# Kernel optimization log

Measured on AMD Instinct MI355X. Metric: run time of the kernel, lower is better.

## Reference

```python
import jax, jax.numpy as jnp
import numpy as np

B = 131072   # batch
K = 3        # kernel size (= stride)
NP = 9       # num patches (9x9 image, 3x3 kernel, stride 3)
NU = 81      # num logic units/kernels
NOPS = 16    # real-valued binary logic ops


def setup_inputs() -> dict:
    key = jax.random.key(0)
    k1, k2, k3, k4 = jax.random.split(key, 4)
    x = jax.random.uniform(k1, (B, 1, 9, 9), dtype=jnp.float32)          # soft-binary image
    sel_a_logits = jax.random.normal(k2, (NU, K * K), dtype=jnp.float32)  # input-A selector per unit
    sel_b_logits = jax.random.normal(k3, (NU, K * K), dtype=jnp.float32)  # input-B selector per unit
    op_logits = jax.random.normal(k4, (NU, NOPS), dtype=jnp.float32)      # logic-op mixture per unit
    return {"x": x, "sel_a_logits": sel_a_logits, "sel_b_logits": sel_b_logits, "op_logits": op_logits}


def _soft_logic_mix(a, b, w):
    # a, b: [B, NU] soft-binary operands; w: [NU, 16] op mixture weights (broadcast over batch).
    # The 16 real-valued binary logic gates (Petersen et al. differentiable logic networks).
    ab = a * b
    return (w[:, 1] * ab
            + w[:, 2] * (a - ab)
            + w[:, 3] * a
            + w[:, 4] * (b - ab)
            + w[:, 5] * b
            + w[:, 6] * (a + b - 2.0 * ab)      # xor
            + w[:, 7] * (a + b - ab)            # or
            + w[:, 8] * (1.0 - (a + b - ab))    # nor
            + w[:, 9] * (1.0 - (a + b - 2.0 * ab))  # xnor
            + w[:, 10] * (1.0 - b)
            + w[:, 11] * (1.0 - b + ab)
            + w[:, 12] * (1.0 - a)
            + w[:, 13] * (1.0 - a + ab)
            + w[:, 14] * (1.0 - ab)             # nand
            + w[:, 15])                          # op 0 contributes 0


def reference(x, sel_a_logits, sel_b_logits, op_logits):
    b_sz = x.shape[0]
    img = x[:, 0]  # [B, 9, 9]
    # unfold(2,K,S).unfold(3,K,S) with S == K == 3 -> non-overlapping 3x3 patches, row-major patch order
    patches = img.reshape(b_sz, NP // K, K, NP // K, K)
    patches = patches.transpose(0, 1, 3, 2, 4).reshape(b_sz, NP, K * K)  # [B, 9, 9]
    # unit u uses patch u // kernels_per_pos (kernels_per_pos = 81 // 9 = 9)
    unit2patch = jnp.arange(NU) // (NU // NP)
    inp = patches[:, unit2patch]  # [B, 81, 9]
    a = jnp.einsum('bui,ui->bu', inp, jax.nn.softmax(sel_a_logits, axis=-1))  # [B, 81]
    b = jnp.einsum('bui,ui->bu', inp, jax.nn.softmax(sel_b_logits, axis=-1))  # [B, 81]
    w = jax.nn.softmax(op_logits, axis=-1)  # [81, 16]
    return _soft_logic_mix(a, b, w)  # [B, 81]
```

## Files before the change

### kernel.cpp

```cpp
#include <hip/hip_runtime.h>
#include <math.h>


#define NB      131072
#define NUNITS  81
#define BPB     64
#define THREADS 256
#define NTILES  (NB / BPB)
#define PBLK    1792
#define REC     24
#define CHUNKS  (BPB * 81 / 4)

typedef __attribute__((address_space(1))) const void GAS;
typedef __attribute__((address_space(3))) void LAS;
typedef float vfloat4 __attribute__((ext_vector_type(4)));

__global__ __launch_bounds__(256)
void logic_prep_kernel(const float* __restrict__ sa_logits,
                       const float* __restrict__ sb_logits,
                       const float* __restrict__ op_logits,
                       float* __restrict__ tab)
{
    const int tid = threadIdx.x;
    if (tid < 81) {
        const int u = tid;
        float v[9], m = -1e30f;
        #pragma unroll
        for (int i = 0; i < 9; ++i) { v[i] = sa_logits[u * 9 + i]; m = fmaxf(m, v[i]); }
        float s = 0.f;
        #pragma unroll
        for (int i = 0; i < 9; ++i) { v[i] = expf(v[i] - m); s += v[i]; }
        const float r = 1.f / s;
        #pragma unroll
        for (int i = 0; i < 9; ++i) tab[u * REC + i] = v[i] * r;
    } else if (tid < 162) {
        const int u = tid - 81;
        float v[9], m = -1e30f;
        #pragma unroll
        for (int i = 0; i < 9; ++i) { v[i] = sb_logits[u * 9 + i]; m = fmaxf(m, v[i]); }
        float s = 0.f;
        #pragma unroll
        for (int i = 0; i < 9; ++i) { v[i] = expf(v[i] - m); s += v[i]; }
        const float r = 1.f / s;
        #pragma unroll
        for (int i = 0; i < 9; ++i) tab[u * REC + 9 + i] = v[i] * r;
    } else if (tid < 243) {
        const int u = tid - 162;
        float v[16], m = -1e30f;
        #pragma unroll
        for (int i = 0; i < 16; ++i) { v[i] = op_logits[u * 16 + i]; m = fmaxf(m, v[i]); }
        float s = 0.f;
        #pragma unroll
        for (int i = 0; i < 16; ++i) { v[i] = expf(v[i] - m); s += v[i]; }
        const float r = 1.f / s;
        #pragma unroll
        for (int i = 0; i < 16; ++i) v[i] *= r;
        const float cab = v[1] - v[2] - v[4] - 2.f*v[6] - v[7] + v[8] + 2.f*v[9]
                        + v[11] + v[13] - v[14];
        const float ca  = v[2] + v[3] + v[6] + v[7] - v[8] - v[9] - v[12] - v[13];
        const float cb  = v[4] + v[5] + v[6] + v[7] - v[8] - v[9] - v[10] - v[11];
        const float c0  = v[8] + v[9] + v[10] + v[11] + v[12] + v[13] + v[14] + v[15];
        tab[u * REC + 18] = cab;
        tab[u * REC + 19] = ca;
        tab[u * REC + 20] = cb;
        tab[u * REC + 21] = c0;
    }
}

__global__ __launch_bounds__(THREADS, 7)
void logic_main_kernel(const float* __restrict__ x,
                       const float* __restrict__ tab,
                       float* __restrict__ out)
{
    __shared__ float s_tile[BPB * 81];

    const int tid   = threadIdx.x;
    const int lane  = tid & 63;
    const int wavei = __builtin_amdgcn_readfirstlane(tid >> 6);

    for (int t = blockIdx.x; t < NTILES; t += PBLK) {
        const size_t b0 = (size_t)t * BPB;

        {
            const float4* gsrc = (const float4*)(x + b0 * 81);
            #pragma unroll
            for (int k = 0; k < 6; ++k) {
                const int j = tid + k * THREADS;
                if (j < CHUNKS) {
                    float* lbase = s_tile + (size_t)(k * THREADS + wavei * 64) * 4;
                    __builtin_amdgcn_global_load_lds((GAS*)(gsrc + j), (LAS*)lbase,
                                                     16, 0, 0);
                }
            }
        }
        __syncthreads();

        if (wavei < 3) {
            float* my = s_tile + lane * 81 + wavei * 27;

            float in[27];
            #pragma unroll
            for (int j = 0; j < 27; ++j) in[j] = my[j];

            const float4* __restrict__ wt4 =
                (const float4*)(tab + (size_t)wavei * 27 * REC);

            #pragma unroll
            for (int j = 0; j < 27; ++j) {
                const int q = j / 9;
                const float4 q0 = wt4[j * 6 + 0];
                const float4 q1 = wt4[j * 6 + 1];
                const float4 q2 = wt4[j * 6 + 2];
                const float4 q3 = wt4[j * 6 + 3];
                const float4 q4 = wt4[j * 6 + 4];
                const float4 q5 = wt4[j * 6 + 5];
                const float wa[9] = { q0.x, q0.y, q0.z, q0.w, q1.x, q1.y, q1.z, q1.w, q2.x };
                const float wb[9] = { q2.y, q2.z, q2.w, q3.x, q3.y, q3.z, q3.w, q4.x, q4.y };
                float a = 0.f, b = 0.f;
                #pragma unroll
                for (int i = 0; i < 9; ++i) {
                    const float xi = in[q * 3 + (i / 3) * 9 + (i % 3)];
                    a = fmaf(xi, wa[i], a);
                    b = fmaf(xi, wb[i], b);
                }
                my[j] = fmaf(q4.z, a * b, fmaf(q4.w, a, fmaf(q5.x, b, q5.y)));
            }
        }

        __syncthreads();

        {
            const vfloat4* s4 = (const vfloat4*)s_tile;
            vfloat4* gdst = (vfloat4*)(out + b0 * 81);
            #pragma unroll
            for (int k = 0; k < 6; ++k) {
                const int j = tid + k * THREADS;
                if (j < CHUNKS) __builtin_nontemporal_store(s4[j], gdst + j);
            }
        }

        __syncthreads();
    }
}

extern "C" void kernel_launch(void* const* d_in, const int* in_sizes, int n_in,
                              void* d_out, int out_size, void* d_ws, size_t ws_size,
                              hipStream_t stream)
{
    const float* x  = (const float*)d_in[0];
    const float* sa = (const float*)d_in[1];
    const float* sb = (const float*)d_in[2];
    const float* op = (const float*)d_in[3];
    float* tab  = (float*)d_ws;
    float* outp = (float*)d_out;

    logic_prep_kernel<<<1, 256, 0, stream>>>(sa, sb, op, tab);
    logic_main_kernel<<<PBLK, THREADS, 0, stream>>>(x, tab, outp);
}
```

Before: 26.37 us.

## Fuse softmax prep into main kernel with flag-based cross-block sync

Merges the single-block table-prep kernel into the main kernel. Block 0 computes the softmax table and publishes it via a release-store flag, while every block issues its input tile load first and then spins on the flag before computing. The goal is to hide one kernel-launch boundary and the prep latency behind the input load. The cost is an extra memset on the stream, a spin-wait that relies on block 0 being scheduled, and a hardcoded tile assignment (last 256 blocks take a second tile) that only works for the fixed NTILES/PBLK values.

After: 80.00 us. +203.3%, slower.

```diff
diff --git a/kernel.cpp b/kernel.cpp
--- a/kernel.cpp
+++ b/kernel.cpp
@@ -10,136 +10,165 @@
 #define PBLK    1792
 #define REC     24
 #define CHUNKS  (BPB * 81 / 4)
+#define TABF    (NUNITS * REC)
 
 typedef __attribute__((address_space(1))) const void GAS;
 typedef __attribute__((address_space(3))) void LAS;
 typedef float vfloat4 __attribute__((ext_vector_type(4)));
 
-__global__ __launch_bounds__(256)
-void logic_prep_kernel(const float* __restrict__ sa_logits,
-                       const float* __restrict__ sb_logits,
-                       const float* __restrict__ op_logits,
-                       float* __restrict__ tab)
+__device__ __forceinline__
+void stage_tile(const float* __restrict__ x, float* __restrict__ s_tile,
+                int tid, int wavei, size_t b0)
 {
-    const int tid = threadIdx.x;
-    if (tid < 81) {
-        const int u = tid;
-        float v[9], m = -1e30f;
+    const float4* gsrc = (const float4*)(x + b0 * 81);
+    #pragma unroll
+    for (int k = 0; k < 6; ++k) {
+        const int j = tid + k * THREADS;
+        if (j < CHUNKS) {
+            float* lbase = s_tile + (size_t)(k * THREADS + wavei * 64) * 4;
+            __builtin_amdgcn_global_load_lds((GAS*)(gsrc + j), (LAS*)lbase,
+                                             16, 0, 0);
+        }
+    }
+}
+
+__device__ __forceinline__
+void compute_tile(float* __restrict__ s_tile, const float* __restrict__ tab,
+                  int lane, int wavei)
+{
+    if (wavei < 3) {
+        float* my = s_tile + lane * 81 + wavei * 27;
+
+        float in[27];
         #pragma unroll
-        for (int i = 0; i < 9; ++i) { v[i] = sa_logits[u * 9 + i]; m = fmaxf(m, v[i]); }
-        float s = 0.f;
+        for (int j = 0; j < 27; ++j) in[j] = my[j];
+
+        const float4* __restrict__ wt4 =
+            (const float4*)(tab + (size_t)wavei * 27 * REC);
+
         #pragma unroll
-        for (int i = 0; i < 9; ++i) { v[i] = expf(v[i] - m); s += v[i]; }
-        const float r = 1.f / s;
-        #pragma unroll
-        for (int i = 0; i < 9; ++i) tab[u * REC + i] = v[i] * r;
-    } else if (tid < 162) {
-        const int u = tid - 81;
-        float v[9], m = -1e30f;
-        #pragma unroll
-        for (int i = 0; i < 9; ++i) { v[i] = sb_logits[u * 9 + i]; m = fmaxf(m, v[i]); }
-        float s = 0.f;
-        #pragma unroll
-        for (int i = 0; i < 9; ++i) { v[i] = expf(v[i] - m); s += v[i]; }
-        const float r = 1.f / s;
-        #pragma unroll
-        for (int i = 0; i < 9; ++i) tab[u * REC + 9 + i] = v[i] * r;
-    } else if (tid < 243) {
-        const int u = tid - 162;
-        float v[16], m = -1e30f;
-        #pragma unroll
-        for (int i = 0; i < 16; ++i) { v[i] = op_logits[u * 16 + i]; m = fmaxf(m, v[i]); }
-        float s = 0.f;
-        #pragma unroll
-        for (int i = 0; i < 16; ++i) { v[i] = expf(v[i] - m); s += v[i]; }
-        const float r = 1.f / s;
-        #pragma unroll
-        for (int i = 0; i < 16; ++i) v[i] *= r;
-        const float cab = v[1] - v[2] - v[4] - 2.f*v[6] - v[7] + v[8] + 2.f*v[9]
-                        + v[11] + v[13] - v[14];
-        const float ca  = v[2] + v[3] + v[6] + v[7] - v[8] - v[9] - v[12] - v[13];
-        const float cb  = v[4] + v[5] + v[6] + v[7] - v[8] - v[9] - v[10] - v[11];
-        const float c0  = v[8] + v[9] + v[10] + v[11] + v[12] + v[13] + v[14] + v[15];
-        tab[u * REC + 18] = cab;
-        tab[u * REC + 19] = ca;
-        tab[u * REC + 20] = cb;
-        tab[u * REC + 21] = c0;
+        for (int j = 0; j < 27; ++j) {
+            const int q = j / 9;
+            const float4 q0 = wt4[j * 6 + 0];
+            const float4 q1 = wt4[j * 6 + 1];
+            const float4 q2 = wt4[j * 6 + 2];
+            const float4 q3 = wt4[j * 6 + 3];
+            const float4 q4 = wt4[j * 6 + 4];
+            const float4 q5 = wt4[j * 6 + 5];
+            const float wa[9] = { q0.x, q0.y, q0.z, q0.w, q1.x, q1.y, q1.z, q1.w, q2.x };
+            const float wb[9] = { q2.y, q2.z, q2.w, q3.x, q3.y, q3.z, q3.w, q4.x, q4.y };
+            float a = 0.f, b = 0.f;
+            #pragma unroll
+            for (int i = 0; i < 9; ++i) {
+                const float xi = in[q * 3 + (i / 3) * 9 + (i % 3)];
+                a = fmaf(xi, wa[i], a);
+                b = fmaf(xi, wb[i], b);
+            }
+            my[j] = fmaf(q4.z, a * b, fmaf(q4.w, a, fmaf(q5.x, b, q5.y)));
+        }
+    }
+}
+
+__device__ __forceinline__
+void writeback_tile(const float* __restrict__ s_tile, float* __restrict__ out,
+                    int tid, size_t b0)
+{
+    const vfloat4* s4 = (const vfloat4*)s_tile;
+    vfloat4* gdst = (vfloat4*)(out + b0 * 81);
+    #pragma unroll
+    for (int k = 0; k < 6; ++k) {
+        const int j = tid + k * THREADS;
+        if (j < CHUNKS) __builtin_nontemporal_store(s4[j], gdst + j);
     }
 }
 
 __global__ __launch_bounds__(THREADS, 7)
-void logic_main_kernel(const float* __restrict__ x,
-                       const float* __restrict__ tab,
-                       float* __restrict__ out)
+void logic_all_kernel(const float* __restrict__ x,
+                      const float* __restrict__ sa_logits,
+                      const float* __restrict__ sb_logits,
+                      const float* __restrict__ op_logits,
+                      float* __restrict__ tab,
+                      int* __restrict__ flag,
+                      float* __restrict__ out)
 {
     __shared__ float s_tile[BPB * 81];
 
     const int tid   = threadIdx.x;
     const int lane  = tid & 63;
     const int wavei = __builtin_amdgcn_readfirstlane(tid >> 6);
+    const int bid   = blockIdx.x;
 
-    for (int t = blockIdx.x; t < NTILES; t += PBLK) {
-        const size_t b0 = (size_t)t * BPB;
-
-        {
-            const float4* gsrc = (const float4*)(x + b0 * 81);
+    if (bid == 0) {
+        if (tid < 81) {
+            const int u = tid;
+            float v[9], m = -1e30f;
             #pragma unroll
-            for (int k = 0; k < 6; ++k) {
-                const int j = tid + k * THREADS;
-                if (j < CHUNKS) {
-                    float* lbase = s_tile + (size_t)(k * THREADS + wavei * 64) * 4;
-                    __builtin_amdgcn_global_load_lds((GAS*)(gsrc + j), (LAS*)lbase,
-                                                     16, 0, 0);
-                }
-            }
+            for (int i = 0; i < 9; ++i) { v[i] = sa_logits[u * 9 + i]; m = fmaxf(m, v[i]); }
+            float s = 0.f;
+            #pragma unroll
+            for (int i = 0; i < 9; ++i) { v[i] = expf(v[i] - m); s += v[i]; }
+            const float r = 1.f / s;
+            #pragma unroll
+            for (int i = 0; i < 9; ++i) tab[u * REC + i] = v[i] * r;
+        } else if (tid < 162) {
+            const int u = tid - 81;
+            float v[9], m = -1e30f;
+            #pragma unroll
+            for (int i = 0; i < 9; ++i) { v[i] = sb_logits[u * 9 + i]; m = fmaxf(m, v[i]); }
+            float s = 0.f;
+            #pragma unroll
+            for (int i = 0; i < 9; ++i) { v[i] = expf(v[i] - m); s += v[i]; }
+            const float r = 1.f / s;
+            #pragma unroll
+            for (int i = 0; i < 9; ++i) tab[u * REC + 9 + i] = v[i] * r;
+        } else if (tid < 243) {
+            const int u = tid - 162;
+            float v[16], m = -1e30f;
+            #pragma unroll
+            for (int i = 0; i < 16; ++i) { v[i] = op_logits[u * 16 + i]; m = fmaxf(m, v[i]); }
+            float s = 0.f;
+            #pragma unroll
+            for (int i = 0; i < 16; ++i) { v[i] = expf(v[i] - m); s += v[i]; }
+            const float r = 1.f / s;
+            #pragma unroll
+            for (int i = 0; i < 16; ++i) v[i] *= r;
+            const float cab = v[1] - v[2] - v[4] - 2.f*v[6] - v[7] + v[8] + 2.f*v[9]
+                            + v[11] + v[13] - v[14];
+            const float ca  = v[2] + v[3] + v[6] + v[7] - v[8] - v[9] - v[12] - v[13];
+            const float cb  = v[4] + v[5] + v[6] + v[7] - v[8] - v[9] - v[10] - v[11];
+            const float c0  = v[8] + v[9] + v[10] + v[11] + v[12] + v[13] + v[14] + v[15];
+            tab[u * REC + 18] = cab;
+            tab[u * REC + 19] = ca;
+            tab[u * REC + 20] = cb;
+            tab[u * REC + 21] = c0;
         }
         __syncthreads();
+        if (tid == 0)
+            __hip_atomic_store(flag, 1, __ATOMIC_RELEASE, __HIP_MEMORY_SCOPE_AGENT);
+    }
 
-        if (wavei < 3) {
-            float* my = s_tile + lane * 81 + wavei * 27;
+    stage_tile(x, s_tile, tid, wavei, (size_t)bid * BPB);
+    __syncthreads();
 
-            float in[27];
-            #pragma unroll
-            for (int j = 0; j < 27; ++j) in[j] = my[j];
+    if (tid == 0) {
+        while (__hip_atomic_load(flag, __ATOMIC_ACQUIRE,
+                                 __HIP_MEMORY_SCOPE_AGENT) == 0)
+            __builtin_amdgcn_s_sleep(8);
+    }
+    __syncthreads();
 
-            const float4* __restrict__ wt4 =
-                (const float4*)(tab + (size_t)wavei * 27 * REC);
+    compute_tile(s_tile, tab, lane, wavei);
+    __syncthreads();
+    writeback_tile(s_tile, out, tid, (size_t)bid * BPB);
 
-            #pragma unroll
-            for (int j = 0; j < 27; ++j) {
-                const int q = j / 9;
-                const float4 q0 = wt4[j * 6 + 0];
-                const float4 q1 = wt4[j * 6 + 1];
-                const float4 q2 = wt4[j * 6 + 2];
-                const float4 q3 = wt4[j * 6 + 3];
-                const float4 q4 = wt4[j * 6 + 4];
-                const float4 q5 = wt4[j * 6 + 5];
-                const float wa[9] = { q0.x, q0.y, q0.z, q0.w, q1.x, q1.y, q1.z, q1.w, q2.x };
-                const float wb[9] = { q2.y, q2.z, q2.w, q3.x, q3.y, q3.z, q3.w, q4.x, q4.y };
-                float a = 0.f, b = 0.f;
-                #pragma unroll
-                for (int i = 0; i < 9; ++i) {
-                    const float xi = in[q * 3 + (i / 3) * 9 + (i % 3)];
-                    a = fmaf(xi, wa[i], a);
-                    b = fmaf(xi, wb[i], b);
-                }
-                my[j] = fmaf(q4.z, a * b, fmaf(q4.w, a, fmaf(q5.x, b, q5.y)));
-            }
-        }
-
+    if (bid >= PBLK - 256) {
         __syncthreads();
-
-        {
-            const vfloat4* s4 = (const vfloat4*)s_tile;
-            vfloat4* gdst = (vfloat4*)(out + b0 * 81);
-            #pragma unroll
-            for (int k = 0; k < 6; ++k) {
-                const int j = tid + k * THREADS;
-                if (j < CHUNKS) __builtin_nontemporal_store(s4[j], gdst + j);
-            }
-        }
-
+        const size_t b1 = (size_t)(bid + 256) * BPB;
+        stage_tile(x, s_tile, tid, wavei, b1);
         __syncthreads();
+        compute_tile(s_tile, tab, lane, wavei);
+        __syncthreads();
+        writeback_tile(s_tile, out, tid, b1);
     }
 }
 
@@ -152,8 +181,9 @@
     const float* sb = (const float*)d_in[2];
     const float* op = (const float*)d_in[3];
     float* tab  = (float*)d_ws;
+    int*   flag = (int*)((float*)d_ws + TABF);
     float* outp = (float*)d_out;
 
-    logic_prep_kernel<<<1, 256, 0, stream>>>(sa, sb, op, tab);
-    logic_main_kernel<<<PBLK, THREADS, 0, stream>>>(x, tab, outp);
+    hipMemsetAsync(flag, 0, sizeof(int), stream);
+    logic_all_kernel<<<PBLK, THREADS, 0, stream>>>(x, sa, sb, op, tab, flag, outp);
 }
```

## Fuse softmax prep into main kernel with per-block LDS weights and smaller tiles

Applied to the files above, without the earlier changes.

Drops the separate single-block prep kernel. Each block now computes the softmax selector and op-mixture coefficients itself into shared memory on its first tile, overlapping that work with the first tile's async global-to-LDS load. The batch tile shrinks from 64 to 48 rows, which gives 2731 tiles and a partial last tile. Weights are read from LDS instead of global memory. The cost is that every block recomputes the exp/softmax work, and the trailing barrier moves to the top of the loop.

Result: slower. 43.05 us (+63.2%).

```diff
diff --git a/kernel.cpp b/kernel.cpp
--- a/kernel.cpp
+++ b/kernel.cpp
@@ -4,126 +4,123 @@
 
 #define NB      131072
 #define NUNITS  81
-#define BPB     64
+#define BPB     48
 #define THREADS 256
-#define NTILES  (NB / BPB)
+#define NTILES  2731
 #define PBLK    1792
-#define REC     24
-#define CHUNKS  (BPB * 81 / 4)
+#define WREC    22
+#define LASTB   (NB - (NTILES - 1) * BPB)
 
 typedef __attribute__((address_space(1))) const void GAS;
 typedef __attribute__((address_space(3))) void LAS;
 typedef float vfloat4 __attribute__((ext_vector_type(4)));
 
-__global__ __launch_bounds__(256)
-void logic_prep_kernel(const float* __restrict__ sa_logits,
-                       const float* __restrict__ sb_logits,
-                       const float* __restrict__ op_logits,
-                       float* __restrict__ tab)
-{
-    const int tid = threadIdx.x;
-    if (tid < 81) {
-        const int u = tid;
-        float v[9], m = -1e30f;
-        #pragma unroll
-        for (int i = 0; i < 9; ++i) { v[i] = sa_logits[u * 9 + i]; m = fmaxf(m, v[i]); }
-        float s = 0.f;
-        #pragma unroll
-        for (int i = 0; i < 9; ++i) { v[i] = expf(v[i] - m); s += v[i]; }
-        const float r = 1.f / s;
-        #pragma unroll
-        for (int i = 0; i < 9; ++i) tab[u * REC + i] = v[i] * r;
-    } else if (tid < 162) {
-        const int u = tid - 81;
-        float v[9], m = -1e30f;
-        #pragma unroll
-        for (int i = 0; i < 9; ++i) { v[i] = sb_logits[u * 9 + i]; m = fmaxf(m, v[i]); }
-        float s = 0.f;
-        #pragma unroll
-        for (int i = 0; i < 9; ++i) { v[i] = expf(v[i] - m); s += v[i]; }
-        const float r = 1.f / s;
-        #pragma unroll
-        for (int i = 0; i < 9; ++i) tab[u * REC + 9 + i] = v[i] * r;
-    } else if (tid < 243) {
-        const int u = tid - 162;
-        float v[16], m = -1e30f;
-        #pragma unroll
-        for (int i = 0; i < 16; ++i) { v[i] = op_logits[u * 16 + i]; m = fmaxf(m, v[i]); }
-        float s = 0.f;
-        #pragma unroll
-        for (int i = 0; i < 16; ++i) { v[i] = expf(v[i] - m); s += v[i]; }
-        const float r = 1.f / s;
-        #pragma unroll
-        for (int i = 0; i < 16; ++i) v[i] *= r;
-        const float cab = v[1] - v[2] - v[4] - 2.f*v[6] - v[7] + v[8] + 2.f*v[9]
-                        + v[11] + v[13] - v[14];
-        const float ca  = v[2] + v[3] + v[6] + v[7] - v[8] - v[9] - v[12] - v[13];
-        const float cb  = v[4] + v[5] + v[6] + v[7] - v[8] - v[9] - v[10] - v[11];
-        const float c0  = v[8] + v[9] + v[10] + v[11] + v[12] + v[13] + v[14] + v[15];
-        tab[u * REC + 18] = cab;
-        tab[u * REC + 19] = ca;
-        tab[u * REC + 20] = cb;
-        tab[u * REC + 21] = c0;
-    }
-}
-
 __global__ __launch_bounds__(THREADS, 7)
-void logic_main_kernel(const float* __restrict__ x,
-                       const float* __restrict__ tab,
-                       float* __restrict__ out)
+void logic_fused_kernel(const float* __restrict__ x,
+                        const float* __restrict__ sa_logits,
+                        const float* __restrict__ sb_logits,
+                        const float* __restrict__ op_logits,
+                        float* __restrict__ out)
 {
     __shared__ float s_tile[BPB * 81];
+    __shared__ float s_w[NUNITS * WREC];
 
     const int tid   = threadIdx.x;
     const int lane  = tid & 63;
     const int wavei = __builtin_amdgcn_readfirstlane(tid >> 6);
+    const int bid   = blockIdx.x;
 
-    for (int t = blockIdx.x; t < NTILES; t += PBLK) {
-        const size_t b0 = (size_t)t * BPB;
+    bool first = true;
+    for (int t = bid; t < NTILES; t += PBLK) {
+        const int nb      = (t == NTILES - 1) ? LASTB : BPB;
+        const int nchunks = nb * 81 / 4;
+        const size_t b0   = (size_t)t * BPB;
+
+        if (!first) __syncthreads();
 
         {
             const float4* gsrc = (const float4*)(x + b0 * 81);
             #pragma unroll
-            for (int k = 0; k < 6; ++k) {
+            for (int k = 0; k < 4; ++k) {
                 const int j = tid + k * THREADS;
-                if (j < CHUNKS) {
+                if (j < nchunks) {
                     float* lbase = s_tile + (size_t)(k * THREADS + wavei * 64) * 4;
                     __builtin_amdgcn_global_load_lds((GAS*)(gsrc + j), (LAS*)lbase,
                                                      16, 0, 0);
                 }
             }
         }
+
+        if (first) {
+            first = false;
+            if (tid < 81) {
+                const int u = tid;
+                float v[9], m = -1e30f;
+                #pragma unroll
+                for (int i = 0; i < 9; ++i) { v[i] = sa_logits[u * 9 + i]; m = fmaxf(m, v[i]); }
+                float s = 0.f;
+                #pragma unroll
+                for (int i = 0; i < 9; ++i) { v[i] = expf(v[i] - m); s += v[i]; }
+                const float r = 1.f / s;
+                #pragma unroll
+                for (int i = 0; i < 9; ++i) s_w[u * WREC + i] = v[i] * r;
+            } else if (tid < 162) {
+                const int u = tid - 81;
+                float v[9], m = -1e30f;
+                #pragma unroll
+                for (int i = 0; i < 9; ++i) { v[i] = sb_logits[u * 9 + i]; m = fmaxf(m, v[i]); }
+                float s = 0.f;
+                #pragma unroll
+                for (int i = 0; i < 9; ++i) { v[i] = expf(v[i] - m); s += v[i]; }
+                const float r = 1.f / s;
+                #pragma unroll
+                for (int i = 0; i < 9; ++i) s_w[u * WREC + 9 + i] = v[i] * r;
+            } else if (tid < 243) {
+                const int u = tid - 162;
+                float v[16], m = -1e30f;
+                #pragma unroll
+                for (int i = 0; i < 16; ++i) { v[i] = op_logits[u * 16 + i]; m = fmaxf(m, v[i]); }
+                float s = 0.f;
+                #pragma unroll
+                for (int i = 0; i < 16; ++i) { v[i] = expf(v[i] - m); s += v[i]; }
+                const float r = 1.f / s;
+                #pragma unroll
+                for (int i = 0; i < 16; ++i) v[i] *= r;
+                const float cab = v[1] - v[2] - v[4] - 2.f*v[6] - v[7] + v[8] + 2.f*v[9]
+                                + v[11] + v[13] - v[14];
+                const float ca  = v[2] + v[3] + v[6] + v[7] - v[8] - v[9] - v[12] - v[13];
+                const float cb  = v[4] + v[5] + v[6] + v[7] - v[8] - v[9] - v[10] - v[11];
+                const float c0  = v[8] + v[9] + v[10] + v[11] + v[12] + v[13] + v[14] + v[15];
+                s_w[u * WREC + 18] = cab;
+                s_w[u * WREC + 19] = ca;
+                s_w[u * WREC + 20] = cb;
+                s_w[u * WREC + 21] = c0;
+            }
+        }
+
         __syncthreads();
 
-        if (wavei < 3) {
+        if (wavei < 3 && lane < nb) {
             float* my = s_tile + lane * 81 + wavei * 27;
 
             float in[27];
             #pragma unroll
             for (int j = 0; j < 27; ++j) in[j] = my[j];
 
-            const float4* __restrict__ wt4 =
-                (const float4*)(tab + (size_t)wavei * 27 * REC);
+            const float* __restrict__ wt = s_w + wavei * 27 * WREC;
 
             #pragma unroll
             for (int j = 0; j < 27; ++j) {
                 const int q = j / 9;
-                const float4 q0 = wt4[j * 6 + 0];
-                const float4 q1 = wt4[j * 6 + 1];
-                const float4 q2 = wt4[j * 6 + 2];
-                const float4 q3 = wt4[j * 6 + 3];
-                const float4 q4 = wt4[j * 6 + 4];
-                const float4 q5 = wt4[j * 6 + 5];
-                const float wa[9] = { q0.x, q0.y, q0.z, q0.w, q1.x, q1.y, q1.z, q1.w, q2.x };
-                const float wb[9] = { q2.y, q2.z, q2.w, q3.x, q3.y, q3.z, q3.w, q4.x, q4.y };
+                const float* __restrict__ wr = wt + j * WREC;
                 float a = 0.f, b = 0.f;
                 #pragma unroll
                 for (int i = 0; i < 9; ++i) {
                     const float xi = in[q * 3 + (i / 3) * 9 + (i % 3)];
-                    a = fmaf(xi, wa[i], a);
-                    b = fmaf(xi, wb[i], b);
+                    a = fmaf(xi, wr[i],     a);
+                    b = fmaf(xi, wr[9 + i], b);
                 }
-                my[j] = fmaf(q4.z, a * b, fmaf(q4.w, a, fmaf(q5.x, b, q5.y)));
+                my[j] = fmaf(wr[18], a * b, fmaf(wr[19], a, fmaf(wr[20], b, wr[21])));
             }
         }
 
@@ -133,13 +130,11 @@
             const vfloat4* s4 = (const vfloat4*)s_tile;
             vfloat4* gdst = (vfloat4*)(out + b0 * 81);
             #pragma unroll
-            for (int k = 0; k < 6; ++k) {
+            for (int k = 0; k < 4; ++k) {
                 const int j = tid + k * THREADS;
-                if (j < CHUNKS) __builtin_nontemporal_store(s4[j], gdst + j);
+                if (j < nchunks) __builtin_nontemporal_store(s4[j], gdst + j);
             }
         }
-
-        __syncthreads();
     }
 }
 
@@ -151,9 +146,7 @@
     const float* sa = (const float*)d_in[1];
     const float* sb = (const float*)d_in[2];
     const float* op = (const float*)d_in[3];
-    float* tab  = (float*)d_ws;
     float* outp = (float*)d_out;
 
-    logic_prep_kernel<<<1, 256, 0, stream>>>(sa, sb, op, tab);
-    logic_main_kernel<<<PBLK, THREADS, 0, stream>>>(x, tab, outp);
+    logic_fused_kernel<<<PBLK, THREADS, 0, stream>>>(x, sa, sb, op, outp);
 }
```
